# Kernel tuning notes

Measured on AMD Instinct MI355X. Metric: run time of the kernel, lower is better.

## Reference

```python
import jax, jax.numpy as jnp
import numpy as np

U, I, D, L = 100000, 100000, 64, 50
B, T = 4096, 100


def setup_inputs() -> dict:
    key = jax.random.key(0)
    ks = jax.random.split(key, 12)
    inp = {}
    inp["item_seq"] = jax.random.randint(ks[0], (B, L), 0, I, dtype=jnp.int64 if jax.config.jax_enable_x64 else jnp.int32)
    inp["user_ids"] = jax.random.randint(ks[1], (B,), 0, U, dtype=jnp.int32)
    inp["items_to_predict"] = jax.random.randint(ks[2], (B, T), 0, I, dtype=jnp.int32)
    # parameters (match torch inits: N(0, 1/d) embeddings, xavier gates, zero b2)
    inp["user_emb_table"] = jax.random.normal(ks[3], (U, D), jnp.float32) / D
    inp["item_emb_table"] = jax.random.normal(ks[4], (I, D), jnp.float32) / D
    lin_s = float(np.sqrt(1.0 / D))
    inp["fg_item_W"] = jax.random.uniform(ks[5], (D, D), jnp.float32, -lin_s, lin_s)
    inp["fg_item_b"] = jax.random.uniform(ks[6], (D,), jnp.float32, -lin_s, lin_s)
    inp["fg_user_W"] = jax.random.uniform(ks[7], (D, D), jnp.float32, -lin_s, lin_s)
    inp["fg_user_b"] = jax.random.uniform(ks[8], (D,), jnp.float32, -lin_s, lin_s)
    xg1 = float(np.sqrt(6.0 / (D + 1)))
    xg2 = float(np.sqrt(6.0 / (D + L)))
    inp["instance_gate_item"] = jax.random.uniform(ks[9], (D, 1), jnp.float32, -xg1, xg1)
    inp["instance_gate_user"] = jax.random.uniform(ks[10], (D, L), jnp.float32, -xg2, xg2)
    W2 = jax.random.normal(ks[11], (I, D), jnp.float32) / D
    inp["W2_table"] = W2.at[0].set(0.0)  # padding_idx=0
    inp["b2_table"] = jnp.zeros((I, 1), jnp.float32)
    return inp


def reference(item_seq, user_ids, items_to_predict, user_emb_table, item_emb_table,
              fg_item_W, fg_item_b, fg_user_W, fg_user_b,
              instance_gate_item, instance_gate_user, W2_table, b2_table):
    item_embs = item_emb_table[item_seq]          # [B, L, D]
    user_emb = user_emb_table[user_ids]           # [B, D]
    # feature gating
    gate = jax.nn.sigmoid(item_embs @ fg_item_W + fg_item_b
                          + (user_emb @ fg_user_W + fg_user_b)[:, None, :])
    gated_item = item_embs * gate                 # [B, L, D]
    # instance gating
    instance_score = jax.nn.sigmoid(
        jnp.einsum('bld,d->bl', gated_item, instance_gate_item[:, 0])
        + user_emb @ instance_gate_user)          # [B, L]
    union_out = jnp.sum(gated_item * instance_score[..., None], axis=1)
    union_out = union_out / jnp.sum(instance_score, axis=1, keepdims=True)  # [B, D]
    # scoring (for_pred=False branch)
    w2 = W2_table[items_to_predict]               # [B, T, D]
    b2 = b2_table[items_to_predict][..., 0]       # [B, T]
    res = b2 + jnp.einsum('btd,bd->bt', w2, user_emb)
    res = res + jnp.einsum('btd,bd->bt', w2, union_out)
    # rel_score: sum_l item_embs @ w2^T == (sum_l item_embs) . w2
    res = res + jnp.einsum('bd,btd->bt', item_embs.sum(axis=1), w2)
    return res
```

## Files before the change

### kernel.cpp

```cpp
#include <hip/hip_runtime.h>

#define D_ 64
#define L_ 50
#define B_ 4096
#define T_ 100
#define SP2 66
#define RS 72

typedef __attribute__((ext_vector_type(8))) short  short8;
typedef __attribute__((ext_vector_type(8))) unsigned short ushort8;
typedef __attribute__((ext_vector_type(4))) float  float4v;
typedef __attribute__((ext_vector_type(4))) unsigned short ushort4v;

__device__ __forceinline__ float sigmoidf_(float x) {
    return 1.0f / (1.0f + __expf(-x));
}
__device__ __forceinline__ unsigned short f2bf(float x) {
    unsigned u = __builtin_bit_cast(unsigned, x);
    return (unsigned short)((u + 0x7fffu + ((u >> 16) & 1u)) >> 16);
}
__device__ __forceinline__ float bf2f(unsigned short s) {
    return __builtin_bit_cast(float, (unsigned)s << 16);
}

__global__ __launch_bounds__(256) void hgn_prep(
    const float4* __restrict__ w2f, ushort8* __restrict__ w2bf,
    const float* __restrict__ fgiW, unsigned short* __restrict__ wbT)
{
    const int bid = blockIdx.x;
    if (bid < 3125) {
        const int j = bid * 256 + threadIdx.x;
        const float4 xa = w2f[2 * j], ya = w2f[2 * j + 1];
        ushort8 oa = { f2bf(xa.x), f2bf(xa.y), f2bf(xa.z), f2bf(xa.w),
                       f2bf(ya.x), f2bf(ya.y), f2bf(ya.z), f2bf(ya.w) };
        w2bf[j] = oa;
    } else {
        const int i = (bid - 3125) * 256 + threadIdx.x;
        if (i < 4096) {
            const int k = i >> 6, c = i & 63;
            wbT[c * 64 + k] = f2bf(fgiW[i]);
        }
    }
}

__global__ __launch_bounds__(256) void hgn_transpose_w(
    const float* __restrict__ fg_item_W, unsigned short* __restrict__ wbT)
{
    const int i = blockIdx.x * 256 + threadIdx.x;
    const int k = i >> 6, c = i & 63;
    wbT[c * 64 + k] = f2bf(fg_item_W[i]);
}

__global__ __launch_bounds__(256) void hgn_fused_main(
    const int* __restrict__ item_seq,
    const int* __restrict__ user_ids,
    const int* __restrict__ items_to_predict,
    const float* __restrict__ user_emb_table,
    const float* __restrict__ item_emb_table,
    const unsigned short* __restrict__ wbT,
    const float* __restrict__ fg_item_b,
    const float* __restrict__ fg_user_W,
    const float* __restrict__ fg_user_b,
    const float* __restrict__ ig_item,
    const float* __restrict__ ig_user,
    const unsigned short* __restrict__ w2bf,
    const float* __restrict__ b2,
    float* __restrict__ out)
{
    __shared__ unsigned short eb_sh[64 * RS];
    __shared__ unsigned short part_sh[L_ * SP2];
    __shared__ __align__(16) float u_sh[D_];
    __shared__ __align__(16) float v_sh[D_];
    __shared__ float gb_sh[D_];
    __shared__ float s_sh[L_];

    const int t    = threadIdx.x;
    const int lane = t & 63;
    const int wave = t >> 6;
    const int b    = blockIdx.x;

    short8 w2r0, w2r1, w2r2, w2r3;
    float b2v = 0.f;
    const int tt = t >> 1, half = t & 1;
    if (t < 2 * T_) {
        const int idxp = items_to_predict[b * T_ + tt];
        const unsigned short* wr = w2bf + (size_t)idxp * D_ + half * 32;
        w2r0 = *(const short8*)(wr + 0);
        w2r1 = *(const short8*)(wr + 8);
        w2r2 = *(const short8*)(wr + 16);
        w2r3 = *(const short8*)(wr + 24);
        b2v  = b2[idxp];
    }

    if (wave == 3) {
        const int uid = user_ids[b];
        u_sh[lane] = user_emb_table[(size_t)uid * D_ + lane];
        float g0 = fg_item_b[lane], g1 = fg_user_b[lane], g2 = 0.f, g3 = 0.f;
#pragma unroll
        for (int k = 0; k < D_; k += 4) {
            g0 = fmaf(u_sh[k + 0], fg_user_W[(k + 0) * D_ + lane], g0);
            g1 = fmaf(u_sh[k + 1], fg_user_W[(k + 1) * D_ + lane], g1);
            g2 = fmaf(u_sh[k + 2], fg_user_W[(k + 2) * D_ + lane], g2);
            g3 = fmaf(u_sh[k + 3], fg_user_W[(k + 3) * D_ + lane], g3);
        }
        gb_sh[lane] = (g0 + g1) + (g2 + g3);
    } else {
        const int tl = t;
#pragma unroll
        for (int r = 0; r < 5; ++r) {
            const int i = tl + 192 * r;
            if (i < L_ * 16) {
                const int l = i >> 4, qd = i & 15;
                const int idx = item_seq[b * L_ + l];
                const float4 e4 = ((const float4*)(item_emb_table + (size_t)idx * D_))[qd];
                ushort4v o = { f2bf(e4.x), f2bf(e4.y), f2bf(e4.z), f2bf(e4.w) };
                *(ushort4v*)&eb_sh[l * RS + qd * 4] = o;
            }
        }
    }
    __syncthreads();

    {
        const int m = lane & 15, q = lane >> 4;
        const int arow = 16 * wave + m;
        const short8 a0 = *(const short8*)&eb_sh[arow * RS + q * 8];
        const short8 a1 = *(const short8*)&eb_sh[arow * RS + 32 + q * 8];
#pragma unroll
        for (int n = 0; n < 4; ++n) {
            const int col = 16 * n + m;
            const short8 b0 = *(const short8*)&wbT[col * 64 + q * 8];
            const short8 b1 = *(const short8*)&wbT[col * 64 + 32 + q * 8];
            float4v acc = {0.f, 0.f, 0.f, 0.f};
            acc = __builtin_amdgcn_mfma_f32_16x16x32_bf16(a0, b0, acc, 0, 0, 0);
            acc = __builtin_amdgcn_mfma_f32_16x16x32_bf16(a1, b1, acc, 0, 0, 0);
            const float gbc = gb_sh[col];
#pragma unroll
            for (int r = 0; r < 4; ++r) {
                const int l = 16 * wave + q * 4 + r;
                if (l < L_) {
                    const float e = bf2f(eb_sh[l * RS + col]);
                    part_sh[l * SP2 + col] = f2bf(e * sigmoidf_(acc[r] + gbc));
                }
            }
        }
    }
    __syncthreads();

    if (lane < L_) {
        float p0 = 0.f, p1 = 0.f, p2 = 0.f, p3 = 0.f;
#pragma unroll
        for (int d = 0; d < D_; d += 4) {
            p0 = fmaf(bf2f(part_sh[lane * SP2 + d + 0]), ig_item[d + 0], p0);
            p1 = fmaf(bf2f(part_sh[lane * SP2 + d + 1]), ig_item[d + 1], p1);
            p2 = fmaf(bf2f(part_sh[lane * SP2 + d + 2]), ig_item[d + 2], p2);
            p3 = fmaf(bf2f(part_sh[lane * SP2 + d + 3]), ig_item[d + 3], p3);
            p0 = fmaf(u_sh[d + 0], ig_user[(d + 0) * L_ + lane], p0);
            p1 = fmaf(u_sh[d + 1], ig_user[(d + 1) * L_ + lane], p1);
            p2 = fmaf(u_sh[d + 2], ig_user[(d + 2) * L_ + lane], p2);
            p3 = fmaf(u_sh[d + 3], ig_user[(d + 3) * L_ + lane], p3);
        }
        s_sh[lane] = sigmoidf_((p0 + p1) + (p2 + p3));
    }
    {
        float e0 = 0.f, e1 = 0.f;
#pragma unroll
        for (int l = 0; l < L_; l += 2) {
            e0 += bf2f(eb_sh[l * RS + lane]);
            e1 += bf2f(eb_sh[(l + 1) * RS + lane]);
        }
        float a0 = 0.f, a1 = 0.f, ss = 0.f;
        for (int l = 0; l < L_; l += 2) {
            const float sA = s_sh[l], sB = s_sh[l + 1];
            a0 = fmaf(bf2f(part_sh[l * SP2 + lane]), sA, a0);
            a1 = fmaf(bf2f(part_sh[(l + 1) * SP2 + lane]), sB, a1);
            ss += sA + sB;
        }
        v_sh[lane] = u_sh[lane] + (a0 + a1) / ss + (e0 + e1);
    }

    if (t < 2 * T_) {
        const float* vh = v_sh + half * 32;
        float a0 = 0.f, a1 = 0.f, a2 = 0.f, a3 = 0.f;
#pragma unroll
        for (int j = 0; j < 8; ++j) {
            a0 = fmaf(bf2f((unsigned short)w2r0[j]), vh[j + 0],  a0);
            a1 = fmaf(bf2f((unsigned short)w2r1[j]), vh[j + 8],  a1);
            a2 = fmaf(bf2f((unsigned short)w2r2[j]), vh[j + 16], a2);
            a3 = fmaf(bf2f((unsigned short)w2r3[j]), vh[j + 24], a3);
        }
        float r = (a0 + a1) + (a2 + a3);
        r += __shfl_xor(r, 1, 64);
        if (half == 0) out[b * T_ + tt] = r + b2v;
    }
}

__global__ __launch_bounds__(256) void hgn_fused_fallback(
    const int* __restrict__ item_seq, const int* __restrict__ user_ids,
    const int* __restrict__ items_to_predict,
    const float* __restrict__ user_emb_table, const float* __restrict__ item_emb_table,
    const unsigned short* __restrict__ wbT, const float* __restrict__ fg_item_b,
    const float* __restrict__ fg_user_W, const float* __restrict__ fg_user_b,
    const float* __restrict__ ig_item, const float* __restrict__ ig_user,
    const float* __restrict__ W2, const float* __restrict__ b2,
    float* __restrict__ out)
{
    __shared__ unsigned short eb_sh[64 * RS];
    __shared__ unsigned short part_sh[L_ * SP2];
    __shared__ __align__(16) float u_sh[D_];
    __shared__ __align__(16) float v_sh[D_];
    __shared__ float gb_sh[D_];
    __shared__ float s_sh[L_];

    const int t = threadIdx.x, lane = t & 63, wave = t >> 6, b = blockIdx.x;

    if (wave == 3) {
        const int uid = user_ids[b];
        u_sh[lane] = user_emb_table[(size_t)uid * D_ + lane];
        float g0 = fg_item_b[lane], g1 = fg_user_b[lane], g2 = 0.f, g3 = 0.f;
#pragma unroll
        for (int k = 0; k < D_; k += 4) {
            g0 = fmaf(u_sh[k + 0], fg_user_W[(k + 0) * D_ + lane], g0);
            g1 = fmaf(u_sh[k + 1], fg_user_W[(k + 1) * D_ + lane], g1);
            g2 = fmaf(u_sh[k + 2], fg_user_W[(k + 2) * D_ + lane], g2);
            g3 = fmaf(u_sh[k + 3], fg_user_W[(k + 3) * D_ + lane], g3);
        }
        gb_sh[lane] = (g0 + g1) + (g2 + g3);
    } else {
#pragma unroll
        for (int r = 0; r < 5; ++r) {
            const int i = t + 192 * r;
            if (i < L_ * 16) {
                const int l = i >> 4, qd = i & 15;
                const int idx = item_seq[b * L_ + l];
                const float4 e4 = ((const float4*)(item_emb_table + (size_t)idx * D_))[qd];
                ushort4v o = { f2bf(e4.x), f2bf(e4.y), f2bf(e4.z), f2bf(e4.w) };
                *(ushort4v*)&eb_sh[l * RS + qd * 4] = o;
            }
        }
    }
    __syncthreads();
    {
        const int m = lane & 15, q = lane >> 4;
        const int arow = 16 * wave + m;
        const short8 a0 = *(const short8*)&eb_sh[arow * RS + q * 8];
        const short8 a1 = *(const short8*)&eb_sh[arow * RS + 32 + q * 8];
#pragma unroll
        for (int n = 0; n < 4; ++n) {
            const int col = 16 * n + m;
            const short8 b0 = *(const short8*)&wbT[col * 64 + q * 8];
            const short8 b1 = *(const short8*)&wbT[col * 64 + 32 + q * 8];
            float4v acc = {0.f, 0.f, 0.f, 0.f};
            acc = __builtin_amdgcn_mfma_f32_16x16x32_bf16(a0, b0, acc, 0, 0, 0);
            acc = __builtin_amdgcn_mfma_f32_16x16x32_bf16(a1, b1, acc, 0, 0, 0);
            const float gbc = gb_sh[col];
#pragma unroll
            for (int r = 0; r < 4; ++r) {
                const int l = 16 * wave + q * 4 + r;
                if (l < L_) {
                    const float e = bf2f(eb_sh[l * RS + col]);
                    part_sh[l * SP2 + col] = f2bf(e * sigmoidf_(acc[r] + gbc));
                }
            }
        }
    }
    __syncthreads();
    if (lane < L_) {
        float p0 = 0.f, p1 = 0.f, p2 = 0.f, p3 = 0.f;
#pragma unroll
        for (int d = 0; d < D_; d += 4) {
            p0 = fmaf(bf2f(part_sh[lane * SP2 + d + 0]), ig_item[d + 0], p0);
            p1 = fmaf(bf2f(part_sh[lane * SP2 + d + 1]), ig_item[d + 1], p1);
            p2 = fmaf(bf2f(part_sh[lane * SP2 + d + 2]), ig_item[d + 2], p2);
            p3 = fmaf(bf2f(part_sh[lane * SP2 + d + 3]), ig_item[d + 3], p3);
            p0 = fmaf(u_sh[d + 0], ig_user[(d + 0) * L_ + lane], p0);
            p1 = fmaf(u_sh[d + 1], ig_user[(d + 1) * L_ + lane], p1);
            p2 = fmaf(u_sh[d + 2], ig_user[(d + 2) * L_ + lane], p2);
            p3 = fmaf(u_sh[d + 3], ig_user[(d + 3) * L_ + lane], p3);
        }
        s_sh[lane] = sigmoidf_((p0 + p1) + (p2 + p3));
    }
    {
        float e0 = 0.f, e1 = 0.f;
#pragma unroll
        for (int l = 0; l < L_; l += 2) {
            e0 += bf2f(eb_sh[l * RS + lane]);
            e1 += bf2f(eb_sh[(l + 1) * RS + lane]);
        }
        float a0 = 0.f, a1 = 0.f, ss = 0.f;
        for (int l = 0; l < L_; l += 2) {
            const float sA = s_sh[l], sB = s_sh[l + 1];
            a0 = fmaf(bf2f(part_sh[l * SP2 + lane]), sA, a0);
            a1 = fmaf(bf2f(part_sh[(l + 1) * SP2 + lane]), sB, a1);
            ss += sA + sB;
        }
        v_sh[lane] = u_sh[lane] + (a0 + a1) / ss + (e0 + e1);
    }
    if (t < 2 * T_) {
        const int tt = t >> 1, half = t & 1;
        const int idx = items_to_predict[b * T_ + tt];
        const float* wrow  = W2 + (size_t)idx * D_ + half * 32;
        const float* vhalf = v_sh + half * 32;
        float r0 = 0.f, r1 = 0.f, r2 = 0.f, r3 = 0.f;
#pragma unroll
        for (int kk = 0; kk < 8; ++kk) {
            const float4 w4 = ((const float4*)wrow)[kk];
            const float4 v4 = ((const float4*)vhalf)[kk];
            r0 = fmaf(v4.x, w4.x, r0);
            r1 = fmaf(v4.y, w4.y, r1);
            r2 = fmaf(v4.z, w4.z, r2);
            r3 = fmaf(v4.w, w4.w, r3);
        }
        float r = (r0 + r1) + (r2 + r3);
        r += __shfl_xor(r, 1, 64);
        if (half == 0) out[b * T_ + tt] = r + b2[idx];
    }
}

extern "C" void kernel_launch(void* const* d_in, const int* in_sizes, int n_in,
                              void* d_out, int out_size, void* d_ws, size_t ws_size,
                              hipStream_t stream) {
    const int*   item_seq   = (const int*)d_in[0];
    const int*   user_ids   = (const int*)d_in[1];
    const int*   items_pred = (const int*)d_in[2];
    const float* uet        = (const float*)d_in[3];
    const float* iet        = (const float*)d_in[4];
    const float* fgiW       = (const float*)d_in[5];
    const float* fgib       = (const float*)d_in[6];
    const float* fguW       = (const float*)d_in[7];
    const float* fgub       = (const float*)d_in[8];
    const float* igi        = (const float*)d_in[9];
    const float* igu        = (const float*)d_in[10];
    const float* W2         = (const float*)d_in[11];
    const float* b2t        = (const float*)d_in[12];

    const size_t tbl_bytes = (size_t)100000 * 64 * 2;
    const size_t need = tbl_bytes + 8192;

    if (ws_size >= need) {
        unsigned short* w2bf = (unsigned short*)d_ws;
        unsigned short* wbT  = (unsigned short*)((char*)d_ws + tbl_bytes);
        hgn_prep<<<3125 + 16, 256, 0, stream>>>(
            (const float4*)W2, (ushort8*)w2bf, fgiW, wbT);
        hgn_fused_main<<<B_, 256, 0, stream>>>(
            item_seq, user_ids, items_pred, uet, iet, wbT,
            fgib, fguW, fgub, igi, igu, w2bf, b2t, (float*)d_out);
    } else {
        unsigned short* wbT = (unsigned short*)d_ws;
        hgn_transpose_w<<<16, 256, 0, stream>>>(fgiW, wbT);
        hgn_fused_fallback<<<B_, 256, 0, stream>>>(
            item_seq, user_ids, items_pred, uet, iet,
            wbT, fgib, fguW, fgub, igi, igu, W2, b2t, (float*)d_out);
    }
}
```

Baseline: 173.2 us.

## Precompute bf16 item table and user gate bias in prep kernel

The prep kernel now also converts the whole item embedding table to bf16 and computes the per-batch user feature-gate bias (user_emb @ fg_user_W + biases) into workspace. The main kernel gathers 16-byte bf16 rows instead of fp32 rows, and no longer runs the 64x64 matvec in wave 3. The instance-score dot product is split across two waves, and the embedding sum moves to a third wave, with an extra barrier. The cost is converting a full 100k-row table every call (a 25.6MB read plus a 12.8MB write), even though only about 205k rows are gathered, and one more barrier.

Result: faster. 168.5 us (-2.7%).

```diff
diff --git a/kernel.cpp b/kernel.cpp
--- a/kernel.cpp
+++ b/kernel.cpp
@@ -24,22 +24,45 @@
 }
 
 __global__ __launch_bounds__(256) void hgn_prep(
-    const float4* __restrict__ w2f, ushort8* __restrict__ w2bf,
-    const float* __restrict__ fgiW, unsigned short* __restrict__ wbT)
+    const float4* __restrict__ w2f, const float4* __restrict__ ietf,
+    ushort8* __restrict__ w2bf, ushort8* __restrict__ ebf,
+    const float* __restrict__ fgiW, unsigned short* __restrict__ wbT,
+    const int* __restrict__ user_ids, const float* __restrict__ user_emb_table,
+    const float* __restrict__ fg_item_b, const float* __restrict__ fg_user_W,
+    const float* __restrict__ fg_user_b, float* __restrict__ gb)
 {
     const int bid = blockIdx.x;
     if (bid < 3125) {
         const int j = bid * 256 + threadIdx.x;
-        const float4 xa = w2f[2 * j], ya = w2f[2 * j + 1];
+        const float4 xa = w2f[2 * j],  ya = w2f[2 * j + 1];
+        const float4 xb = ietf[2 * j], yb = ietf[2 * j + 1];
         ushort8 oa = { f2bf(xa.x), f2bf(xa.y), f2bf(xa.z), f2bf(xa.w),
                        f2bf(ya.x), f2bf(ya.y), f2bf(ya.z), f2bf(ya.w) };
+        ushort8 ob = { f2bf(xb.x), f2bf(xb.y), f2bf(xb.z), f2bf(xb.w),
+                       f2bf(yb.x), f2bf(yb.y), f2bf(yb.z), f2bf(yb.w) };
         w2bf[j] = oa;
-    } else {
+        ebf[j]  = ob;
+    } else if (bid < 3141) {
         const int i = (bid - 3125) * 256 + threadIdx.x;
         if (i < 4096) {
             const int k = i >> 6, c = i & 63;
             wbT[c * 64 + k] = f2bf(fgiW[i]);
         }
+    } else {
+        const int wave = threadIdx.x >> 6, lane = threadIdx.x & 63;
+        const int b = (bid - 3141) * 4 + wave;
+        const int uid = user_ids[b];
+        const float* urow = user_emb_table + (size_t)uid * D_;
+        float g0 = fg_item_b[lane], g1 = fg_user_b[lane], g2 = 0.f, g3 = 0.f;
+#pragma unroll
+        for (int kk = 0; kk < 16; ++kk) {
+            const float4 u4 = ((const float4*)urow)[kk];
+            g0 = fmaf(u4.x, fg_user_W[(4 * kk + 0) * D_ + lane], g0);
+            g1 = fmaf(u4.y, fg_user_W[(4 * kk + 1) * D_ + lane], g1);
+            g2 = fmaf(u4.z, fg_user_W[(4 * kk + 2) * D_ + lane], g2);
+            g3 = fmaf(u4.w, fg_user_W[(4 * kk + 3) * D_ + lane], g3);
+        }
+        gb[b * D_ + lane] = (g0 + g1) + (g2 + g3);
     }
 }
 
@@ -56,11 +79,9 @@
     const int* __restrict__ user_ids,
     const int* __restrict__ items_to_predict,
     const float* __restrict__ user_emb_table,
-    const float* __restrict__ item_emb_table,
+    const unsigned short* __restrict__ ebf,
     const unsigned short* __restrict__ wbT,
-    const float* __restrict__ fg_item_b,
-    const float* __restrict__ fg_user_W,
-    const float* __restrict__ fg_user_b,
+    const float* __restrict__ gb,
     const float* __restrict__ ig_item,
     const float* __restrict__ ig_user,
     const unsigned short* __restrict__ w2bf,
@@ -73,6 +94,8 @@
     __shared__ __align__(16) float v_sh[D_];
     __shared__ float gb_sh[D_];
     __shared__ float s_sh[L_];
+    __shared__ float bp_sh[2][64];
+    __shared__ float esum_sh[D_];
 
     const int t    = threadIdx.x;
     const int lane = t & 63;
@@ -94,29 +117,20 @@
 
     if (wave == 3) {
         const int uid = user_ids[b];
-        u_sh[lane] = user_emb_table[(size_t)uid * D_ + lane];
-        float g0 = fg_item_b[lane], g1 = fg_user_b[lane], g2 = 0.f, g3 = 0.f;
-#pragma unroll
-        for (int k = 0; k < D_; k += 4) {
-            g0 = fmaf(u_sh[k + 0], fg_user_W[(k + 0) * D_ + lane], g0);
-            g1 = fmaf(u_sh[k + 1], fg_user_W[(k + 1) * D_ + lane], g1);
-            g2 = fmaf(u_sh[k + 2], fg_user_W[(k + 2) * D_ + lane], g2);
-            g3 = fmaf(u_sh[k + 3], fg_user_W[(k + 3) * D_ + lane], g3);
-        }
-        gb_sh[lane] = (g0 + g1) + (g2 + g3);
+        u_sh[lane]  = user_emb_table[(size_t)uid * D_ + lane];
+        gb_sh[lane] = gb[b * D_ + lane];
     } else {
-        const int tl = t;
-#pragma unroll
-        for (int r = 0; r < 5; ++r) {
-            const int i = tl + 192 * r;
-            if (i < L_ * 16) {
-                const int l = i >> 4, qd = i & 15;
-                const int idx = item_seq[b * L_ + l];
-                const float4 e4 = ((const float4*)(item_emb_table + (size_t)idx * D_))[qd];
-                ushort4v o = { f2bf(e4.x), f2bf(e4.y), f2bf(e4.z), f2bf(e4.w) };
-                *(ushort4v*)&eb_sh[l * RS + qd * 4] = o;
-            }
-        }
+        const int i0 = t, i1 = t + 192, i2 = t + 384;
+        const int id0 = item_seq[b * L_ + (i0 >> 3)];
+        const int id1 = item_seq[b * L_ + (i1 >> 3)];
+        const int id2 = (i2 < 400) ? item_seq[b * L_ + (i2 >> 3)] : 0;
+        const short8 r0 = *(const short8*)(ebf + (size_t)id0 * D_ + (i0 & 7) * 8);
+        const short8 r1 = *(const short8*)(ebf + (size_t)id1 * D_ + (i1 & 7) * 8);
+        short8 r2;
+        if (i2 < 400) r2 = *(const short8*)(ebf + (size_t)id2 * D_ + (i2 & 7) * 8);
+        *(short8*)&eb_sh[(i0 >> 3) * RS + (i0 & 7) * 8] = r0;
+        *(short8*)&eb_sh[(i1 >> 3) * RS + (i1 & 7) * 8] = r1;
+        if (i2 < 400) *(short8*)&eb_sh[(i2 >> 3) * RS + (i2 & 7) * 8] = r2;
     }
     __syncthreads();
 
@@ -146,28 +160,37 @@
     }
     __syncthreads();
 
-    if (lane < L_) {
-        float p0 = 0.f, p1 = 0.f, p2 = 0.f, p3 = 0.f;
-#pragma unroll
-        for (int d = 0; d < D_; d += 4) {
-            p0 = fmaf(bf2f(part_sh[lane * SP2 + d + 0]), ig_item[d + 0], p0);
-            p1 = fmaf(bf2f(part_sh[lane * SP2 + d + 1]), ig_item[d + 1], p1);
-            p2 = fmaf(bf2f(part_sh[lane * SP2 + d + 2]), ig_item[d + 2], p2);
-            p3 = fmaf(bf2f(part_sh[lane * SP2 + d + 3]), ig_item[d + 3], p3);
-            p0 = fmaf(u_sh[d + 0], ig_user[(d + 0) * L_ + lane], p0);
-            p1 = fmaf(u_sh[d + 1], ig_user[(d + 1) * L_ + lane], p1);
-            p2 = fmaf(u_sh[d + 2], ig_user[(d + 2) * L_ + lane], p2);
-            p3 = fmaf(u_sh[d + 3], ig_user[(d + 3) * L_ + lane], p3);
-        }
-        s_sh[lane] = sigmoidf_((p0 + p1) + (p2 + p3));
-    }
-    {
+    if (wave < 2) {
+        if (lane < L_) {
+            const int d0 = 32 * wave;
+            float p0 = 0.f, p1 = 0.f, p2 = 0.f, p3 = 0.f;
+#pragma unroll
+            for (int j = 0; j < 32; j += 4) {
+                const int d = d0 + j;
+                p0 = fmaf(bf2f(part_sh[lane * SP2 + d + 0]), ig_item[d + 0], p0);
+                p1 = fmaf(bf2f(part_sh[lane * SP2 + d + 1]), ig_item[d + 1], p1);
+                p2 = fmaf(bf2f(part_sh[lane * SP2 + d + 2]), ig_item[d + 2], p2);
+                p3 = fmaf(bf2f(part_sh[lane * SP2 + d + 3]), ig_item[d + 3], p3);
+                p0 = fmaf(u_sh[d + 0], ig_user[(d + 0) * L_ + lane], p0);
+                p1 = fmaf(u_sh[d + 1], ig_user[(d + 1) * L_ + lane], p1);
+                p2 = fmaf(u_sh[d + 2], ig_user[(d + 2) * L_ + lane], p2);
+                p3 = fmaf(u_sh[d + 3], ig_user[(d + 3) * L_ + lane], p3);
+            }
+            bp_sh[wave][lane] = (p0 + p1) + (p2 + p3);
+        }
+    } else if (wave == 2) {
         float e0 = 0.f, e1 = 0.f;
 #pragma unroll
         for (int l = 0; l < L_; l += 2) {
             e0 += bf2f(eb_sh[l * RS + lane]);
             e1 += bf2f(eb_sh[(l + 1) * RS + lane]);
         }
+        esum_sh[lane] = e0 + e1;
+    }
+    __syncthreads();
+
+    if (lane < L_) s_sh[lane] = sigmoidf_(bp_sh[0][lane] + bp_sh[1][lane]);
+    {
         float a0 = 0.f, a1 = 0.f, ss = 0.f;
         for (int l = 0; l < L_; l += 2) {
             const float sA = s_sh[l], sB = s_sh[l + 1];
@@ -175,9 +198,8 @@
             a1 = fmaf(bf2f(part_sh[(l + 1) * SP2 + lane]), sB, a1);
             ss += sA + sB;
         }
-        v_sh[lane] = u_sh[lane] + (a0 + a1) / ss + (e0 + e1);
-    }
-
+        v_sh[lane] = u_sh[lane] + (a0 + a1) / ss + esum_sh[lane];
+    }
     if (t < 2 * T_) {
         const float* vh = v_sh + half * 32;
         float a0 = 0.f, a1 = 0.f, a2 = 0.f, a3 = 0.f;
@@ -210,6 +232,8 @@
     __shared__ __align__(16) float v_sh[D_];
     __shared__ float gb_sh[D_];
     __shared__ float s_sh[L_];
+    __shared__ float bp_sh[2][64];
+    __shared__ float esum_sh[D_];
 
     const int t = threadIdx.x, lane = t & 63, wave = t >> 6, b = blockIdx.x;
 
@@ -264,28 +288,36 @@
         }
     }
     __syncthreads();
-    if (lane < L_) {
-        float p0 = 0.f, p1 = 0.f, p2 = 0.f, p3 = 0.f;
-#pragma unroll
-        for (int d = 0; d < D_; d += 4) {
-            p0 = fmaf(bf2f(part_sh[lane * SP2 + d + 0]), ig_item[d + 0], p0);
-            p1 = fmaf(bf2f(part_sh[lane * SP2 + d + 1]), ig_item[d + 1], p1);
-            p2 = fmaf(bf2f(part_sh[lane * SP2 + d + 2]), ig_item[d + 2], p2);
-            p3 = fmaf(bf2f(part_sh[lane * SP2 + d + 3]), ig_item[d + 3], p3);
-            p0 = fmaf(u_sh[d + 0], ig_user[(d + 0) * L_ + lane], p0);
-            p1 = fmaf(u_sh[d + 1], ig_user[(d + 1) * L_ + lane], p1);
-            p2 = fmaf(u_sh[d + 2], ig_user[(d + 2) * L_ + lane], p2);
-            p3 = fmaf(u_sh[d + 3], ig_user[(d + 3) * L_ + lane], p3);
-        }
-        s_sh[lane] = sigmoidf_((p0 + p1) + (p2 + p3));
-    }
-    {
+    if (wave < 2) {
+        if (lane < L_) {
+            const int d0 = 32 * wave;
+            float p0 = 0.f, p1 = 0.f, p2 = 0.f, p3 = 0.f;
+#pragma unroll
+            for (int j = 0; j < 32; j += 4) {
+                const int d = d0 + j;
+                p0 = fmaf(bf2f(part_sh[lane * SP2 + d + 0]), ig_item[d + 0], p0);
+                p1 = fmaf(bf2f(part_sh[lane * SP2 + d + 1]), ig_item[d + 1], p1);
+                p2 = fmaf(bf2f(part_sh[lane * SP2 + d + 2]), ig_item[d + 2], p2);
+                p3 = fmaf(bf2f(part_sh[lane * SP2 + d + 3]), ig_item[d + 3], p3);
+                p0 = fmaf(u_sh[d + 0], ig_user[(d + 0) * L_ + lane], p0);
+                p1 = fmaf(u_sh[d + 1], ig_user[(d + 1) * L_ + lane], p1);
+                p2 = fmaf(u_sh[d + 2], ig_user[(d + 2) * L_ + lane], p2);
+                p3 = fmaf(u_sh[d + 3], ig_user[(d + 3) * L_ + lane], p3);
+            }
+            bp_sh[wave][lane] = (p0 + p1) + (p2 + p3);
+        }
+    } else if (wave == 2) {
         float e0 = 0.f, e1 = 0.f;
 #pragma unroll
         for (int l = 0; l < L_; l += 2) {
             e0 += bf2f(eb_sh[l * RS + lane]);
             e1 += bf2f(eb_sh[(l + 1) * RS + lane]);
         }
+        esum_sh[lane] = e0 + e1;
+    }
+    __syncthreads();
+    if (lane < L_) s_sh[lane] = sigmoidf_(bp_sh[0][lane] + bp_sh[1][lane]);
+    {
         float a0 = 0.f, a1 = 0.f, ss = 0.f;
         for (int l = 0; l < L_; l += 2) {
             const float sA = s_sh[l], sB = s_sh[l + 1];
@@ -293,7 +325,7 @@
             a1 = fmaf(bf2f(part_sh[(l + 1) * SP2 + lane]), sB, a1);
             ss += sA + sB;
         }
-        v_sh[lane] = u_sh[lane] + (a0 + a1) / ss + (e0 + e1);
+        v_sh[lane] = u_sh[lane] + (a0 + a1) / ss + esum_sh[lane];
     }
     if (t < 2 * T_) {
         const int tt = t >> 1, half = t & 1;
@@ -333,17 +365,23 @@
     const float* W2         = (const float*)d_in[11];
     const float* b2t        = (const float*)d_in[12];
 
-    const size_t tbl_bytes = (size_t)100000 * 64 * 2;
-    const size_t need = tbl_bytes + 8192;
+    const size_t tbl_elems = (size_t)100000 * 64;
+    const size_t tbl_bytes = tbl_elems * 2;
+    const size_t gb_bytes  = (size_t)B_ * D_ * 4;
+    const size_t need = 2 * tbl_bytes + gb_bytes + 8192;
 
     if (ws_size >= need) {
         unsigned short* w2bf = (unsigned short*)d_ws;
-        unsigned short* wbT  = (unsigned short*)((char*)d_ws + tbl_bytes);
-        hgn_prep<<<3125 + 16, 256, 0, stream>>>(
-            (const float4*)W2, (ushort8*)w2bf, fgiW, wbT);
+        unsigned short* ebf  = (unsigned short*)((char*)d_ws + tbl_bytes);
+        float*          gbuf = (float*)((char*)d_ws + 2 * tbl_bytes);
+        unsigned short* wbT  = (unsigned short*)((char*)d_ws + 2 * tbl_bytes + gb_bytes);
+        hgn_prep<<<3125 + 16 + 1024, 256, 0, stream>>>(
+            (const float4*)W2, (const float4*)iet,
+            (ushort8*)w2bf, (ushort8*)ebf, fgiW, wbT,
+            user_ids, uet, fgib, fguW, fgub, gbuf);
         hgn_fused_main<<<B_, 256, 0, stream>>>(
-            item_seq, user_ids, items_pred, uet, iet, wbT,
-            fgib, fguW, fgub, igi, igu, w2bf, b2t, (float*)d_out);
+            item_seq, user_ids, items_pred, uet, ebf, wbT, gbuf,
+            igi, igu, w2bf, b2t, (float*)d_out);
     } else {
         unsigned short* wbT = (unsigned short*)d_ws;
         hgn_transpose_w<<<16, 256, 0, stream>>>(fgiW, wbT);
```
